# Kernel tuning notes

Hardware: AMD Instinct MI355X
Metric: run time of the kernel (lower is better)

Reference implementation:

```python
import jax, jax.numpy as jnp
import numpy as np
from jax import lax

KH, KW, K = 3, 3, 9
PAD, BN_EPS = 1, 1e-5


def setup_inputs() -> dict:
    key = jax.random.key(0)
    ks = jax.random.split(key, 10)
    B, CHI, CHO, H, W = 2, 64, 64, 128, 128
    x = jax.random.normal(ks[0], (B, CHI, H, W), dtype=jnp.float32)
    # offset/mask branch conv: 3*K output channels (o1, o2, mask)
    w_off = jax.random.normal(ks[1], (3 * K, CHI, KH, KW), dtype=jnp.float32) * 0.01
    b_off = jax.random.normal(ks[2], (3 * K,), dtype=jnp.float32) * 0.01
    # main deformable conv weight/bias
    fan = CHI * K
    weight = jax.random.normal(ks[3], (CHO, CHI, KH, KW), dtype=jnp.float32) / np.sqrt(fan)
    bias = jax.random.normal(ks[4], (CHO,), dtype=jnp.float32) * 0.01
    # BatchNorm (eval-mode) params
    gamma = jax.random.uniform(ks[5], (CHO,), minval=0.5, maxval=1.5, dtype=jnp.float32)
    beta = jax.random.normal(ks[6], (CHO,), dtype=jnp.float32) * 0.1
    run_mean = jax.random.normal(ks[7], (CHO,), dtype=jnp.float32) * 0.1
    run_var = jax.random.uniform(ks[8], (CHO,), minval=0.5, maxval=1.5, dtype=jnp.float32)
    return {"x": x, "w_off": w_off, "b_off": b_off, "weight": weight,
            "bias": bias, "gamma": gamma, "beta": beta,
            "run_mean": run_mean, "run_var": run_var}


def _dcn_bn_relu(x, w_off, b_off, weight, bias, gamma, beta, run_mean, run_var):
    B, C, H, W = x.shape
    CHO = weight.shape[0]
    # offset/mask branch: regular 3x3 conv, stride 1, pad 1
    om = lax.conv_general_dilated(
        x, w_off, window_strides=(1, 1), padding=[(PAD, PAD), (PAD, PAD)],
        dimension_numbers=("NCHW", "OIHW", "NCHW")) + b_off[None, :, None, None]
    o1, o2, m = jnp.split(om, 3, axis=1)          # each [B, K, H, W]
    offset = jnp.concatenate([o1, o2], axis=1)    # [B, 2K, H, W]
    off_y = offset[:, 0::2]                       # interleaved (y, x) per tap, as in DCNv2 CUDA
    off_x = offset[:, 1::2]
    mask = jax.nn.sigmoid(m)                      # [B, K, H, W] modulation

    # sampling positions: p = p0 + p_k + offset
    ky, kx = jnp.meshgrid(jnp.arange(KH), jnp.arange(KW), indexing="ij")
    ky = ky.reshape(K).astype(x.dtype)
    kx = kx.reshape(K).astype(x.dtype)
    hh = jnp.arange(H, dtype=x.dtype)
    ww = jnp.arange(W, dtype=x.dtype)
    py = hh[None, None, :, None] - PAD + ky[None, :, None, None] + off_y  # [B,K,H,W]
    px = ww[None, None, None, :] - PAD + kx[None, :, None, None] + off_x

    y0f = jnp.floor(py)
    x0f = jnp.floor(px)
    ly = (py - y0f)[..., None]
    lx = (px - x0f)[..., None]
    y0 = y0f.astype(jnp.int32)
    x0 = x0f.astype(jnp.int32)
    bidx = jnp.arange(B)[:, None, None, None]

    def gather(yi, xi):
        valid = ((yi >= 0) & (yi < H) & (xi >= 0) & (xi < W)).astype(x.dtype)
        yc = jnp.clip(yi, 0, H - 1)
        xc = jnp.clip(xi, 0, W - 1)
        g = x[bidx, :, yc, xc]                    # [B, K, H, W, C]
        return g * valid[..., None]

    v00 = gather(y0, x0)
    v01 = gather(y0, x0 + 1)
    v10 = gather(y0 + 1, x0)
    v11 = gather(y0 + 1, x0 + 1)
    sampled = (v00 * (1 - ly) * (1 - lx) + v01 * (1 - ly) * lx
               + v10 * ly * (1 - lx) + v11 * ly * lx)
    sampled = sampled * mask[..., None]           # modulated

    out = jnp.einsum("bkhwc,ock->bohw", sampled,
                     weight.reshape(CHO, C, K)) + bias[None, :, None, None]

    # eval-mode BatchNorm + ReLU
    inv = gamma / jnp.sqrt(run_var + BN_EPS)
    out = (out - run_mean[None, :, None, None]) * inv[None, :, None, None] \
          + beta[None, :, None, None]
    return jax.nn.relu(out)


def reference(x, w_off, b_off, weight, bias, gamma, beta, run_mean, run_var):
    return _dcn_bn_relu(x, w_off, b_off, weight, bias, gamma, beta, run_mean, run_var)
```

## Files before the change

### kernel.cpp

```cpp
#include <hip/hip_runtime.h>
#include <hip/hip_bf16.h>

#define HH 128
#define WW 128
#define CI 64
#define CO 64
#define SLS 584
#define A_HPS 72
#define A_HW 66

typedef __attribute__((ext_vector_type(8))) short short8;
typedef __attribute__((ext_vector_type(4))) float floatx4;

__device__ __forceinline__ unsigned short f2bf(float f) {
  union { float f; unsigned u; } uu; uu.f = f;
  unsigned r = uu.u + 0x7FFFu + ((uu.u >> 16) & 1u);
  return (unsigned short)(r >> 16);
}
__device__ __forceinline__ unsigned pack2bf(float lo, float hi) {
  return (unsigned)f2bf(lo) | ((unsigned)f2bf(hi) << 16);
}

__global__ __launch_bounds__(256) void prep_kernel(
    const float* __restrict__ weight, const float* __restrict__ bias,
    const float* __restrict__ gamma, const float* __restrict__ beta,
    const float* __restrict__ mean, const float* __restrict__ var,
    const float* __restrict__ w_off, const float* __restrict__ b_off,
    unsigned short* __restrict__ Wm, unsigned short* __restrict__ w2,
    float* __restrict__ bias2, float* __restrict__ boff2) {
  int idx = blockIdx.x * 256 + threadIdx.x;
  if (idx < 32) boff2[idx] = (idx < 27) ? b_off[idx] : 0.f;
  if (idx >= CO * 576) return;
  int o = idx / 576, kc = idx - o * 576;
  int k = kc >> 6, c = kc & 63;
  float inv = gamma[o] * rsqrtf(var[o] + 1e-5f);
  Wm[idx] = f2bf(weight[(o * CI + c) * 9 + k] * inv);
  if (kc == 0) bias2[o] = (bias[o] - mean[o]) * inv + beta[o];
  if (o < 27) w2[idx] = f2bf(w_off[o * 576 + c * 9 + k]);
  else if (o < 32) w2[idx] = 0;
}

__global__ __launch_bounds__(256) void offA_kernel(
    const float* __restrict__ x, unsigned* __restrict__ xTb_u,
    const unsigned short* __restrict__ w2, const float* __restrict__ boff2,
    float* __restrict__ om32) {
  __shared__ short halo[3 * A_HW * A_HPS];
  int bid = blockIdx.x;
  int s = bid & 7;
  int n = bid >> 3;
  int b = n >> 5;
  int rest = n & 31;
  int h = s * 16 + (rest & 15);
  int w0 = (rest >> 4) * 64;
  int tid = threadIdx.x;

#pragma unroll
  for (int it = 0; it < 4; it++) {
    int t = it * 256 + tid;
    if (t < 792) {
      int row = t / 264;
      int r2 = t - row * 264;
      int cg4 = r2 / 66;
      int px = r2 - cg4 * 66;
      int y = h - 1 + row;
      int xi = w0 - 1 + px;
      int c0 = cg4 * 16;
      float f[16];
      if (((unsigned)y < (unsigned)HH) && ((unsigned)xi < (unsigned)WW)) {
        const float* xp = x + ((long)(b * CI + c0) * HH + y) * WW + xi;
#pragma unroll
        for (int q = 0; q < 16; q++) f[q] = xp[q * (HH * WW)];
      } else {
#pragma unroll
        for (int q = 0; q < 16; q++) f[q] = 0.f;
      }
      short* hp = &halo[(row * A_HW + px) * A_HPS + c0];
#pragma unroll
      for (int q = 0; q < 4; q++)
        *(uint2*)(hp + q * 4) =
            make_uint2(pack2bf(f[4 * q], f[4 * q + 1]), pack2bf(f[4 * q + 2], f[4 * q + 3]));
    }
  }
  __syncthreads();

  {
    int cp = tid & 31;
    int pw = tid >> 5;
#pragma unroll
    for (int it = 0; it < 8; it++) {
      int px = it * 8 + pw;
      unsigned u = *(const unsigned*)&halo[(A_HW + px + 1) * A_HPS + 2 * cp];
      xTb_u[((b * HH + h) * WW + w0 + px) * 32 + cp] = u;
    }
  }

  int lane = tid & 63, wave = tid >> 6;
  int r16 = lane & 15, quad = lane >> 4;
  int m16 = wave & 1;
  floatx4 binit = *(const floatx4*)(boff2 + m16 * 16 + quad * 4);
  const short* ap = (const short*)(w2 + (m16 * 16 + r16) * 576);
#pragma unroll
  for (int i = 0; i < 2; i++) {
    int nt = (wave >> 1) + 2 * i;
    floatx4 t = binit;
#pragma unroll
    for (int kk = 0; kk < 9; kk++) {
      int dy = kk / 3, dx = kk - 3 * (kk / 3);
      const short* hp = &halo[(dy * A_HW + nt * 16 + r16 + dx) * A_HPS];
      short8 b0 = *(const short8*)(hp + quad * 8);
      short8 b1 = *(const short8*)(hp + 32 + quad * 8);
      short8 a0 = *(const short8*)(ap + kk * 64 + quad * 8);
      short8 a1 = *(const short8*)(ap + kk * 64 + 32 + quad * 8);
      t = __builtin_amdgcn_mfma_f32_16x16x32_bf16(a0, b0, t, 0, 0, 0);
      t = __builtin_amdgcn_mfma_f32_16x16x32_bf16(a1, b1, t, 0, 0, 0);
    }
    float* orow = om32 + (long)((b * HH + h) * WW + w0 + nt * 16 + r16) * 32;
#pragma unroll
    for (int r = 0; r < 4; r++) {
      int oc = m16 * 16 + quad * 4 + r;
      if (oc < 27) orow[oc] = t[r];
    }
  }
}

__global__ __launch_bounds__(256) void dcnB_kernel(
    const unsigned short* __restrict__ xTb, const float* __restrict__ om32,
    const unsigned short* __restrict__ Wm, const float* __restrict__ bias2,
    float* __restrict__ out) {
  __shared__ __hip_bfloat16 SL[16 * SLS];
  __shared__ float4 Pw[144];
  __shared__ int2 Po[144];

  int bid = blockIdx.x;
  int s = bid & 7;
  int n = bid >> 3;
  int b = n >> 7;
  int rem = n & 127;
  int h = s * 16 + (rem >> 3);
  int w0 = (rem & 7) * 16;

  int tid = threadIdx.x, lane = tid & 63, wave = tid >> 6;
  const unsigned short* xb = xTb + b * (HH * WW * CI);
  int rowpix = (b * HH + h) * WW + w0;

  if (lane < 36) {
    int p_loc = (lane * 7282) >> 16;
    int k = lane - p_loc * 9;
    int p = wave * 4 + p_loc;
    const float* ob = om32 + (long)(rowpix + p) * 32;
    float oy = ob[2 * k], ox = ob[2 * k + 1], mm = ob[18 + k];
    float msk = 1.f / (1.f + __expf(-mm));
    int ky = (k * 11) >> 5;
    int kx = k - 3 * ky;
    float py = (float)(h - 1 + ky) + oy;
    float px = (float)(w0 + p - 1 + kx) + ox;
    float y0f = floorf(py), x0f = floorf(px);
    float ly = py - y0f, lx = px - x0f;
    int y0 = (int)y0f, x0 = (int)x0f;
    int y1 = y0 + 1, x1 = x0 + 1;
    float lylx = ly * lx;
    bool y0v = (unsigned)y0 < (unsigned)HH, y1v = (unsigned)y1 < (unsigned)HH;
    bool x0v = (unsigned)x0 < (unsigned)WW, x1v = (unsigned)x1 < (unsigned)WW;
    int yc0 = min(max(y0, 0), HH - 1), yc1 = min(max(y1, 0), HH - 1);
    int xc0 = min(max(x0, 0), WW - 1), xc1 = min(max(x1, 0), WW - 1);
    Pw[p * 9 + k] = make_float4((y0v && x0v) ? (1.f - ly - lx + lylx) * msk : 0.f,
                                (y0v && x1v) ? (lx - lylx) * msk : 0.f,
                                (y1v && x0v) ? (ly - lylx) * msk : 0.f,
                                (y1v && x1v) ? lylx * msk : 0.f);
    int dxs = (xc1 - xc0) * CI;
    int dys = (yc1 - yc0) * WW * CI;
    Po[p * 9 + k] = make_int2((yc0 * WW + xc0) * CI, dxs | (dys << 16));
  }

  int cp = lane & 31, ph = lane >> 5, ch = 2 * cp;
#pragma unroll
  for (int j = 0; j < 2; j++) {
    int p = wave * 4 + j * 2 + ph;
#pragma unroll
    for (int k = 0; k < 9; k++) {
      float4 wv = Pw[p * 9 + k];
      int2 po = Po[p * 9 + k];
      int o00 = po.x + ch;
      int dx = po.y & 0xffff;
      int dyv = po.y >> 16;
      unsigned u00 = *(const unsigned*)(xb + o00);
      unsigned u01 = *(const unsigned*)(xb + o00 + dx);
      unsigned u10 = *(const unsigned*)(xb + o00 + dyv);
      unsigned u11 = *(const unsigned*)(xb + o00 + dyv + dx);
      float lo = __uint_as_float(u00 << 16) * wv.x + __uint_as_float(u01 << 16) * wv.y +
                 __uint_as_float(u10 << 16) * wv.z + __uint_as_float(u11 << 16) * wv.w;
      float hi = __uint_as_float(u00 & 0xffff0000u) * wv.x + __uint_as_float(u01 & 0xffff0000u) * wv.y +
                 __uint_as_float(u10 & 0xffff0000u) * wv.z + __uint_as_float(u11 & 0xffff0000u) * wv.w;
      *(unsigned*)(&SL[p * SLS + k * 64 + ch]) = pack2bf(lo, hi);
    }
  }
  __syncthreads();

  int r16 = lane & 15, quad = lane >> 4;
  floatx4 acc = *(const floatx4*)(bias2 + wave * 16 + quad * 4);
  const unsigned short* Ap = Wm + (wave * 16 + r16) * 576 + quad * 8;
  const __hip_bfloat16* Sp = &SL[r16 * SLS + quad * 8];
#pragma unroll
  for (int kc0 = 0; kc0 < 576; kc0 += 32) {
    short8 av = *(const short8*)(Ap + kc0);
    short8 bv = *(const short8*)(Sp + kc0);
    acc = __builtin_amdgcn_mfma_f32_16x16x32_bf16(av, bv, acc, 0, 0, 0);
  }
#pragma unroll
  for (int r = 0; r < 4; r++) {
    int o = wave * 16 + quad * 4 + r;
    out[((b * CO + o) * HH + h) * WW + w0 + r16] = fmaxf(acc[r], 0.f);
  }
}

extern "C" void kernel_launch(void* const* d_in, const int* in_sizes, int n_in,
                              void* d_out, int out_size, void* d_ws, size_t ws_size,
                              hipStream_t stream) {
  const float* x = (const float*)d_in[0];
  const float* w_off = (const float*)d_in[1];
  const float* b_off = (const float*)d_in[2];
  const float* weight = (const float*)d_in[3];
  const float* bias = (const float*)d_in[4];
  const float* gamma = (const float*)d_in[5];
  const float* beta = (const float*)d_in[6];
  const float* run_mean = (const float*)d_in[7];
  const float* run_var = (const float*)d_in[8];
  float* outp = (float*)d_out;

  char* ws = (char*)d_ws;
  unsigned* xTb = (unsigned*)ws;
  float* om32 = (float*)(ws + 4194304);
  unsigned short* Wm = (unsigned short*)(ws + 8388608);
  unsigned short* w2 = (unsigned short*)(ws + 8462336);
  float* bias2 = (float*)(ws + 8499200);
  float* boff2 = (float*)(ws + 8499456);

  prep_kernel<<<144, 256, 0, stream>>>(weight, bias, gamma, beta, run_mean, run_var,
                                       w_off, b_off, Wm, w2, bias2, boff2);
  offA_kernel<<<512, 256, 0, stream>>>(x, xTb, w2, boff2, om32);
  dcnB_kernel<<<2048, 256, 0, stream>>>((const unsigned short*)xTb, om32, Wm, bias2, outp);
}
```

Measured before the change: 109.7 us.

## Halve offset-conv tile width and widen bilinear gather to four channels per lane

The offset/mask conv kernel now tiles 32 pixels per block instead of 64, doubling the grid to 1024 blocks with a smaller halo and one MFMA tile per wave. The aim is more parallelism and occupancy, at the cost of more halo re-reads. In the deformable sampling stage, each lane now gathers four bf16 channels with 8-byte loads instead of two with 4-byte loads. This halves the number of gather instructions and processes one pixel per lane group per pass.

```diff
diff --git a/kernel.cpp b/kernel.cpp
--- a/kernel.cpp
+++ b/kernel.cpp
@@ -7,7 +7,7 @@
 #define CO 64
 #define SLS 584
 #define A_HPS 72
-#define A_HW 66
+#define A_HW 34
 
 typedef __attribute__((ext_vector_type(8))) short short8;
 typedef __attribute__((ext_vector_type(4))) float floatx4;
@@ -20,6 +20,8 @@
 __device__ __forceinline__ unsigned pack2bf(float lo, float hi) {
   return (unsigned)f2bf(lo) | ((unsigned)f2bf(hi) << 16);
 }
+__device__ __forceinline__ float bflo(unsigned u) { return __uint_as_float(u << 16); }
+__device__ __forceinline__ float bfhi(unsigned u) { return __uint_as_float(u & 0xffff0000u); }
 
 __global__ __launch_bounds__(256) void prep_kernel(
     const float* __restrict__ weight, const float* __restrict__ bias,
@@ -48,20 +50,20 @@
   int bid = blockIdx.x;
   int s = bid & 7;
   int n = bid >> 3;
-  int b = n >> 5;
-  int rest = n & 31;
-  int h = s * 16 + (rest & 15);
-  int w0 = (rest >> 4) * 64;
+  int b = n >> 6;
+  int rem = n & 63;
+  int h = s * 16 + (rem >> 2);
+  int w0 = (rem & 3) * 32;
   int tid = threadIdx.x;
 
 #pragma unroll
-  for (int it = 0; it < 4; it++) {
+  for (int it = 0; it < 2; it++) {
     int t = it * 256 + tid;
-    if (t < 792) {
-      int row = t / 264;
-      int r2 = t - row * 264;
-      int cg4 = r2 / 66;
-      int px = r2 - cg4 * 66;
+    if (t < 408) {
+      int row = t / 136;
+      int r2 = t - row * 136;
+      int cg4 = r2 / 34;
+      int px = r2 - cg4 * 34;
       int y = h - 1 + row;
       int xi = w0 - 1 + px;
       int c0 = cg4 * 16;
@@ -87,7 +89,7 @@
     int cp = tid & 31;
     int pw = tid >> 5;
 #pragma unroll
-    for (int it = 0; it < 8; it++) {
+    for (int it = 0; it < 4; it++) {
       int px = it * 8 + pw;
       unsigned u = *(const unsigned*)&halo[(A_HW + px + 1) * A_HPS + 2 * cp];
       xTb_u[((b * HH + h) * WW + w0 + px) * 32 + cp] = u;
@@ -97,29 +99,25 @@
   int lane = tid & 63, wave = tid >> 6;
   int r16 = lane & 15, quad = lane >> 4;
   int m16 = wave & 1;
-  floatx4 binit = *(const floatx4*)(boff2 + m16 * 16 + quad * 4);
+  int nt = wave >> 1;
+  floatx4 t = *(const floatx4*)(boff2 + m16 * 16 + quad * 4);
   const short* ap = (const short*)(w2 + (m16 * 16 + r16) * 576);
 #pragma unroll
-  for (int i = 0; i < 2; i++) {
-    int nt = (wave >> 1) + 2 * i;
-    floatx4 t = binit;
-#pragma unroll
-    for (int kk = 0; kk < 9; kk++) {
-      int dy = kk / 3, dx = kk - 3 * (kk / 3);
-      const short* hp = &halo[(dy * A_HW + nt * 16 + r16 + dx) * A_HPS];
-      short8 b0 = *(const short8*)(hp + quad * 8);
-      short8 b1 = *(const short8*)(hp + 32 + quad * 8);
-      short8 a0 = *(const short8*)(ap + kk * 64 + quad * 8);
-      short8 a1 = *(const short8*)(ap + kk * 64 + 32 + quad * 8);
-      t = __builtin_amdgcn_mfma_f32_16x16x32_bf16(a0, b0, t, 0, 0, 0);
-      t = __builtin_amdgcn_mfma_f32_16x16x32_bf16(a1, b1, t, 0, 0, 0);
-    }
-    float* orow = om32 + (long)((b * HH + h) * WW + w0 + nt * 16 + r16) * 32;
-#pragma unroll
-    for (int r = 0; r < 4; r++) {
-      int oc = m16 * 16 + quad * 4 + r;
-      if (oc < 27) orow[oc] = t[r];
-    }
+  for (int kk = 0; kk < 9; kk++) {
+    int dy = kk / 3, dx = kk - 3 * (kk / 3);
+    const short* hp = &halo[(dy * A_HW + nt * 16 + r16 + dx) * A_HPS];
+    short8 b0 = *(const short8*)(hp + quad * 8);
+    short8 b1 = *(const short8*)(hp + 32 + quad * 8);
+    short8 a0 = *(const short8*)(ap + kk * 64 + quad * 8);
+    short8 a1 = *(const short8*)(ap + kk * 64 + 32 + quad * 8);
+    t = __builtin_amdgcn_mfma_f32_16x16x32_bf16(a0, b0, t, 0, 0, 0);
+    t = __builtin_amdgcn_mfma_f32_16x16x32_bf16(a1, b1, t, 0, 0, 0);
+  }
+  float* orow = om32 + (long)((b * HH + h) * WW + w0 + nt * 16 + r16) * 32;
+#pragma unroll
+  for (int r = 0; r < 4; r++) {
+    int oc = m16 * 16 + quad * 4 + r;
+    if (oc < 27) orow[oc] = t[r];
   }
 }
 
@@ -172,26 +170,25 @@
     Po[p * 9 + k] = make_int2((yc0 * WW + xc0) * CI, dxs | (dys << 16));
   }
 
-  int cp = lane & 31, ph = lane >> 5, ch = 2 * cp;
-#pragma unroll
-  for (int j = 0; j < 2; j++) {
-    int p = wave * 4 + j * 2 + ph;
+  {
+    int c4 = (lane & 15) * 4;
+    int p = wave * 4 + (lane >> 4);
 #pragma unroll
     for (int k = 0; k < 9; k++) {
       float4 wv = Pw[p * 9 + k];
       int2 po = Po[p * 9 + k];
-      int o00 = po.x + ch;
+      int o00 = po.x + c4;
       int dx = po.y & 0xffff;
       int dyv = po.y >> 16;
-      unsigned u00 = *(const unsigned*)(xb + o00);
-      unsigned u01 = *(const unsigned*)(xb + o00 + dx);
-      unsigned u10 = *(const unsigned*)(xb + o00 + dyv);
-      unsigned u11 = *(const unsigned*)(xb + o00 + dyv + dx);
-      float lo = __uint_as_float(u00 << 16) * wv.x + __uint_as_float(u01 << 16) * wv.y +
-                 __uint_as_float(u10 << 16) * wv.z + __uint_as_float(u11 << 16) * wv.w;
-      float hi = __uint_as_float(u00 & 0xffff0000u) * wv.x + __uint_as_float(u01 & 0xffff0000u) * wv.y +
-                 __uint_as_float(u10 & 0xffff0000u) * wv.z + __uint_as_float(u11 & 0xffff0000u) * wv.w;
-      *(unsigned*)(&SL[p * SLS + k * 64 + ch]) = pack2bf(lo, hi);
+      uint2 u00 = *(const uint2*)(xb + o00);
+      uint2 u01 = *(const uint2*)(xb + o00 + dx);
+      uint2 u10 = *(const uint2*)(xb + o00 + dyv);
+      uint2 u11 = *(const uint2*)(xb + o00 + dyv + dx);
+      float f0 = bflo(u00.x) * wv.x + bflo(u01.x) * wv.y + bflo(u10.x) * wv.z + bflo(u11.x) * wv.w;
+      float f1 = bfhi(u00.x) * wv.x + bfhi(u01.x) * wv.y + bfhi(u10.x) * wv.z + bfhi(u11.x) * wv.w;
+      float f2 = bflo(u00.y) * wv.x + bflo(u01.y) * wv.y + bflo(u10.y) * wv.z + bflo(u11.y) * wv.w;
+      float f3 = bfhi(u00.y) * wv.x + bfhi(u01.y) * wv.y + bfhi(u10.y) * wv.z + bfhi(u11.y) * wv.w;
+      *(uint2*)(&SL[p * SLS + k * 64 + c4]) = make_uint2(pack2bf(f0, f1), pack2bf(f2, f3));
     }
   }
   __syncthreads();
@@ -237,6 +234,6 @@
 
   prep_kernel<<<144, 256, 0, stream>>>(weight, bias, gamma, beta, run_mean, run_var,
                                        w_off, b_off, Wm, w2, bias2, boff2);
-  offA_kernel<<<512, 256, 0, stream>>>(x, xTb, w2, boff2, om32);
+  offA_kernel<<<1024, 256, 0, stream>>>(x, xTb, w2, boff2, om32);
   dcnB_kernel<<<2048, 256, 0, stream>>>((const unsigned short*)xTb, om32, Wm, bias2, outp);
 }
```

Result: slower. 117.8 us (+7.4%).
